# Kernel tuning notes

Hardware: AMD Instinct MI355X
Metric: run time of the kernel (lower is better)

## Reference

```python
import jax, jax.numpy as jnp
import numpy as np

TEMPERATURE = 0.1
BATCH_SIZE = 64
EPS = 1e-8  # torch.nn.CosineSimilarity eps
NEG_INF = -1e30

B, C, D = 64, 16, 512  # batch, children per sample, feature dim


def setup_inputs() -> dict:
    key = jax.random.key(0)
    k1, k2, k3, k4 = jax.random.split(key, 4)
    children_is = jax.random.normal(k1, (B, C, D), dtype=jnp.float32)
    children_js = jax.random.normal(k2, (B, C, D), dtype=jnp.float32)
    partnet_ids = jnp.arange(B, dtype=jnp.int64 if jax.config.jax_enable_x64 else jnp.int32)
    neg_idx_j = jax.random.randint(k3, (B, B, C), 0, C)  # negatives drawn from children_js
    neg_idx_k = jax.random.randint(k4, (B, B, C), 0, C)  # negatives drawn from children_is
    return {
        "children_is": children_is,
        "children_js": children_js,
        "partnet_ids": partnet_ids,
        "neg_idx_j": neg_idx_j,
        "neg_idx_k": neg_idx_k,
    }


def _safe_norm(x, axis=-1):
    return jnp.maximum(jnp.sqrt(jnp.sum(x * x, axis=axis)), EPS)


def _ntxent(ci, cj, pids, nj, nk):
    b = ci.shape[0]
    fi = ci.reshape(b, -1)  # [B, L] flattened anchors
    fj = cj.reshape(b, -1)  # [B, L] flattened positives
    norm_i = _safe_norm(fi)

    # positive: cos(flat(children_i), flat(children_j[i])) / T
    pos = jnp.sum(fi * fj, axis=-1) / (norm_i * _safe_norm(fj))  # [B]

    src = jnp.arange(b)[None, :, None]  # broadcast source-sample index
    # gathered negatives: g*[i, j] = children_*[j, neg_idx[i, j]] flattened -> [B, B, L]
    gj = cj[src, nj].reshape(b, b, -1)
    gk = ci[src, nk].reshape(b, b, -1)

    sim_j = jnp.einsum('il,ijl->ij', fi, gj) / (norm_i[:, None] * _safe_norm(gj))
    sim_k = jnp.einsum('il,ijl->ij', fi, gk) / (norm_i[:, None] * _safe_norm(gk))

    # negative pair valid iff j != i and partnet ids differ
    eye = jnp.arange(b)
    mask = (eye[None, :] != eye[:, None]) & (pids[None, :] != pids[:, None])  # [B, B]

    logits = jnp.concatenate(
        [pos[:, None],
         jnp.where(mask, sim_j, NEG_INF),
         jnp.where(mask, sim_k, NEG_INF)], axis=1) / TEMPERATURE  # [B, 1+2B]

    # CrossEntropy with label 0, reduction='sum' over the batch of anchors
    loss = jnp.sum(-logits[:, 0] + jax.scipy.special.logsumexp(logits, axis=1))
    return loss / (2.0 * BATCH_SIZE)


def reference(children_is, children_js, partnet_ids, neg_idx_j, neg_idx_k):
    return _ntxent(children_is, children_js, partnet_ids, neg_idx_j, neg_idx_k)
```

## Files before the change

### kernel.cpp

```cpp
#include <hip/hip_runtime.h>
#include <math.h>

#define BB 64
#define CC 16
#define DD 512
#define LL 8192
#define EPSV 1e-8f
#define INVT 10.0f
#define NEGINF_T (-1e31f)

#define OFF_CIB 0u
#define OFF_CJB (1u << 20)
#define BASE2   (2u << 20)
#define OFF_N2I (BASE2)
#define OFF_N2J (BASE2 + 4096u)
#define OFF_POS (BASE2 + 8192u)
#define OFF_DJ  (BASE2 + 12288u)
#define OFF_DK  (BASE2 + 12288u + 16384u)
#define OFF_GJ  (BASE2 + 12288u + 32768u)
#define OFF_GK  (BASE2 + 12288u + 49152u)

typedef short bf16x8 __attribute__((ext_vector_type(8)));
typedef float f32x4  __attribute__((ext_vector_type(4)));

__device__ __forceinline__ float dot4(float4 a, float4 b) {
    return a.x * b.x + a.y * b.y + a.z * b.z + a.w * b.w;
}
__device__ __forceinline__ float wave_reduce(float v) {
    #pragma unroll
    for (int off = 32; off; off >>= 1) v += __shfl_down(v, off);
    return v;
}
__device__ __forceinline__ unsigned short f2bf(float f) {
    union { float f; unsigned u; } x; x.f = f;
    return (unsigned short)((x.u + 0x7fffu + ((x.u >> 16) & 1u)) >> 16);
}

__global__ __launch_bounds__(256) void ntx_prep(const float* __restrict__ ci,
                                                const float* __restrict__ cj,
                                                char* __restrict__ ws,
                                                float* __restrict__ out) {
    const int b = blockIdx.x, tid = threadIdx.x;
    const int wave = tid >> 6, lane = tid & 63;
    __shared__ float red[4];

    if (b < 512) {
        const int r  = b * 4 + wave;
        const int rr = r & 1023;
        const bool is_i = (r < 1024);
        const float* src = is_i ? ci : cj;
        unsigned short* dst = (unsigned short*)(ws + (is_i ? OFF_CIB : OFF_CJB));
        float4 v1 = ((const float4*)(src + rr * DD))[lane];
        float4 v2 = ((const float4*)(src + rr * DD))[64 + lane];
        float acc = wave_reduce(dot4(v1, v1) + dot4(v2, v2));
        if (lane == 0) ((float*)(ws + (is_i ? OFF_N2I : OFF_N2J)))[rr] = acc;
        ushort4 h1 = { f2bf(v1.x), f2bf(v1.y), f2bf(v1.z), f2bf(v1.w) };
        ushort4 h2 = { f2bf(v2.x), f2bf(v2.y), f2bf(v2.z), f2bf(v2.w) };
        ((ushort4*)(dst + rr * DD))[lane]      = h1;
        ((ushort4*)(dst + rr * DD))[64 + lane] = h2;
    } else {
        const int i = b - 512;
        if (b == 512 && tid == 0) out[0] = 0.f;
        const float4* fi = (const float4*)(ci + i * LL);
        const float4* fj = (const float4*)(cj + i * LL);
        float acc = 0.f;
        #pragma unroll
        for (int it = 0; it < 8; ++it) acc += dot4(fi[tid + 256 * it], fj[tid + 256 * it]);
        acc = wave_reduce(acc);
        if (lane == 0) red[wave] = acc;
        __syncthreads();
        if (tid == 0) ((float*)(ws + OFF_POS))[i] = red[0] + red[1] + red[2] + red[3];
    }
}

__global__ __launch_bounds__(256) void ntx_strip(const int* __restrict__ nj,
                                                 const int* __restrict__ nk,
                                                 char* __restrict__ ws) {
    const int b = blockIdx.x;
    const int i = b >> 2, q = b & 3;
    const int side = q >> 1, jh = q & 1;
    const int tid  = threadIdx.x;
    const int wave = tid >> 6, lane = tid & 63;
    const int quad = lane >> 4, lr = lane & 15;

    __shared__ float sS[16][512];

    const short* A  = (const short*)(ws + OFF_CIB) + i * CC * DD;
    const short* Bm = (const short*)(ws + (side ? OFF_CIB : OFF_CJB)) + jh * 512 * DD;

    f32x4 acc[8] = {};
    #pragma unroll
    for (int kk = 0; kk < 16; ++kk) {
        const int k = kk * 32 + quad * 8;
        bf16x8 av = *(const bf16x8*)(A + lr * DD + k);
        #pragma unroll
        for (int tt = 0; tt < 8; ++tt) {
            const int row = (wave * 8 + tt) * 16 + lr;
            bf16x8 bv = *(const bf16x8*)(Bm + row * DD + k);
            acc[tt] = __builtin_amdgcn_mfma_f32_16x16x32_bf16(av, bv, acc[tt], 0, 0, 0);
        }
    }
    #pragma unroll
    for (int tt = 0; tt < 8; ++tt) {
        const int t = wave * 8 + tt;
        #pragma unroll
        for (int r = 0; r < 4; ++r)
            sS[quad * 4 + r][t * 16 + lr] = acc[tt][r];
    }
    __syncthreads();

    const int jj = tid >> 3;
    const int g  = tid & 7;
    const int j  = jh * 32 + jj;
    const int* idxp = (side ? nk : nj) + (i * BB + j) * CC;
    const float* n2 = (const float*)(ws + (side ? OFF_N2I : OFF_N2J)) + j * CC;
    const int c0 = g * 2;
    const int x0 = idxp[c0], x1 = idxp[c0 + 1];
    float d  = sS[c0][jj * 16 + x0] + sS[c0 + 1][jj * 16 + x1];
    float gn = n2[x0] + n2[x1];
    d += __shfl_down(d, 4);  gn += __shfl_down(gn, 4);
    d += __shfl_down(d, 2);  gn += __shfl_down(gn, 2);
    d += __shfl_down(d, 1);  gn += __shfl_down(gn, 1);
    if (g == 0) {
        ((float*)(ws + (side ? OFF_DK : OFF_DJ)))[i * BB + j] = d;
        ((float*)(ws + (side ? OFF_GK : OFF_GJ)))[i * BB + j] = gn;
    }
}

__global__ __launch_bounds__(64) void ntx_final(const int* __restrict__ pids,
                                                const char* __restrict__ ws_c,
                                                float* __restrict__ out) {
    const int i = blockIdx.x, j = threadIdx.x;
    const float* n2i = (const float*)(ws_c + OFF_N2I);
    const float* n2j = (const float*)(ws_c + OFF_N2J);
    const float* pos = (const float*)(ws_c + OFF_POS);

    float si = 0.f, sjf = 0.f;
    #pragma unroll
    for (int c = 0; c < CC; ++c) { si += n2i[i * CC + c]; sjf += n2j[i * CC + c]; }
    const float ni = fmaxf(sqrtf(si), EPSV);
    const float l0 = pos[i] / (ni * fmaxf(sqrtf(sjf), EPSV)) * INVT;

    const float dj = ((const float*)(ws_c + OFF_DJ))[i * BB + j];
    const float dk = ((const float*)(ws_c + OFF_DK))[i * BB + j];
    const float gj = ((const float*)(ws_c + OFF_GJ))[i * BB + j];
    const float gk = ((const float*)(ws_c + OFF_GK))[i * BB + j];

    const bool valid = (j != i) && (pids[j] != pids[i]);
    float lj = NEGINF_T, lk = NEGINF_T;
    if (valid) {
        const float inv = INVT / ni;
        lj = dj / fmaxf(sqrtf(gj), EPSV) * inv;
        lk = dk / fmaxf(sqrtf(gk), EPSV) * inv;
    }

    float m = fmaxf(lj, lk);
    #pragma unroll
    for (int off = 32; off; off >>= 1) m = fmaxf(m, __shfl_xor(m, off));
    m = fmaxf(m, l0);

    float s = __expf(lj - m) + __expf(lk - m);
    s = wave_reduce(s);
    if (j == 0) {
        s += __expf(l0 - m);
        const float loss_i = -l0 + m + __logf(s);
        atomicAdd(out, loss_i * (1.0f / (2.0f * BB)));
    }
}

extern "C" void kernel_launch(void* const* d_in, const int* in_sizes, int n_in,
                              void* d_out, int out_size, void* d_ws, size_t ws_size,
                              hipStream_t stream) {
    const float* ci  = (const float*)d_in[0];
    const float* cj  = (const float*)d_in[1];
    const int*  pids = (const int*) d_in[2];
    const int*  nj   = (const int*) d_in[3];
    const int*  nk   = (const int*) d_in[4];
    char*  ws  = (char*)d_ws;
    float* out = (float*)d_out;

    ntx_prep<<<576, 256, 0, stream>>>(ci, cj, ws, out);
    ntx_strip<<<256, 256, 0, stream>>>(nj, nk, ws);
    ntx_final<<<BB, 64, 0, stream>>>(pids, ws, out);
}
```

Baseline: 86.47 us.

## Fold final loss into strip kernel via last-block counter; fuse positive dot into prep

The separate final kernel is removed. The loss reduction now runs in the last of the four strip blocks per anchor, detected with an atomic counter plus threadfence. The prep kernel handles ci and cj rows together, computing per-row norms, the per-row positive dot product and the bf16 conversion in one pass, so the separate positive-dot blocks are no longer needed. This saves a kernel launch and a pass over the inputs, at the cost of atomic counter traffic and a workspace counter that prep must zero.

```diff
diff --git a/kernel.cpp b/kernel.cpp
--- a/kernel.cpp
+++ b/kernel.cpp
@@ -14,11 +14,12 @@
 #define BASE2   (2u << 20)
 #define OFF_N2I (BASE2)
 #define OFF_N2J (BASE2 + 4096u)
-#define OFF_POS (BASE2 + 8192u)
+#define OFF_PR  (BASE2 + 8192u)
 #define OFF_DJ  (BASE2 + 12288u)
-#define OFF_DK  (BASE2 + 12288u + 16384u)
-#define OFF_GJ  (BASE2 + 12288u + 32768u)
-#define OFF_GK  (BASE2 + 12288u + 49152u)
+#define OFF_DK  (BASE2 + 28672u)
+#define OFF_GJ  (BASE2 + 45056u)
+#define OFF_GK  (BASE2 + 61440u)
+#define OFF_CNT (BASE2 + 77824u)
 
 typedef short bf16x8 __attribute__((ext_vector_type(8)));
 typedef float f32x4  __attribute__((ext_vector_type(4)));
@@ -42,40 +43,42 @@
                                                 float* __restrict__ out) {
     const int b = blockIdx.x, tid = threadIdx.x;
     const int wave = tid >> 6, lane = tid & 63;
-    __shared__ float red[4];
-
-    if (b < 512) {
-        const int r  = b * 4 + wave;
-        const int rr = r & 1023;
-        const bool is_i = (r < 1024);
-        const float* src = is_i ? ci : cj;
-        unsigned short* dst = (unsigned short*)(ws + (is_i ? OFF_CIB : OFF_CJB));
-        float4 v1 = ((const float4*)(src + rr * DD))[lane];
-        float4 v2 = ((const float4*)(src + rr * DD))[64 + lane];
-        float acc = wave_reduce(dot4(v1, v1) + dot4(v2, v2));
-        if (lane == 0) ((float*)(ws + (is_i ? OFF_N2I : OFF_N2J)))[rr] = acc;
-        ushort4 h1 = { f2bf(v1.x), f2bf(v1.y), f2bf(v1.z), f2bf(v1.w) };
-        ushort4 h2 = { f2bf(v2.x), f2bf(v2.y), f2bf(v2.z), f2bf(v2.w) };
-        ((ushort4*)(dst + rr * DD))[lane]      = h1;
-        ((ushort4*)(dst + rr * DD))[64 + lane] = h2;
-    } else {
-        const int i = b - 512;
-        if (b == 512 && tid == 0) out[0] = 0.f;
-        const float4* fi = (const float4*)(ci + i * LL);
-        const float4* fj = (const float4*)(cj + i * LL);
-        float acc = 0.f;
-        #pragma unroll
-        for (int it = 0; it < 8; ++it) acc += dot4(fi[tid + 256 * it], fj[tid + 256 * it]);
-        acc = wave_reduce(acc);
-        if (lane == 0) red[wave] = acc;
-        __syncthreads();
-        if (tid == 0) ((float*)(ws + OFF_POS))[i] = red[0] + red[1] + red[2] + red[3];
+    const int r = b * 4 + wave;
+
+    const float4* ci4 = (const float4*)(ci + r * DD);
+    const float4* cj4 = (const float4*)(cj + r * DD);
+    float4 a1 = ci4[lane], a2 = ci4[64 + lane];
+    float4 b1 = cj4[lane], b2 = cj4[64 + lane];
+
+    float ni = wave_reduce(dot4(a1, a1) + dot4(a2, a2));
+    float nj = wave_reduce(dot4(b1, b1) + dot4(b2, b2));
+    float pd = wave_reduce(dot4(a1, b1) + dot4(a2, b2));
+    if (lane == 0) {
+        ((float*)(ws + OFF_N2I))[r] = ni;
+        ((float*)(ws + OFF_N2J))[r] = nj;
+        ((float*)(ws + OFF_PR))[r]  = pd;
+    }
+
+    ushort4 hi1 = { f2bf(a1.x), f2bf(a1.y), f2bf(a1.z), f2bf(a1.w) };
+    ushort4 hi2 = { f2bf(a2.x), f2bf(a2.y), f2bf(a2.z), f2bf(a2.w) };
+    ushort4 hj1 = { f2bf(b1.x), f2bf(b1.y), f2bf(b1.z), f2bf(b1.w) };
+    ushort4 hj2 = { f2bf(b2.x), f2bf(b2.y), f2bf(b2.z), f2bf(b2.w) };
+    ushort4* di = (ushort4*)((unsigned short*)(ws + OFF_CIB) + r * DD);
+    ushort4* dj = (ushort4*)((unsigned short*)(ws + OFF_CJB) + r * DD);
+    di[lane] = hi1;  di[64 + lane] = hi2;
+    dj[lane] = hj1;  dj[64 + lane] = hj2;
+
+    if (b == 0) {
+        if (tid < 64)       ((int*)(ws + OFF_CNT))[tid] = 0;
+        else if (tid == 64) out[0] = 0.f;
     }
 }
 
 __global__ __launch_bounds__(256) void ntx_strip(const int* __restrict__ nj,
                                                  const int* __restrict__ nk,
-                                                 char* __restrict__ ws) {
+                                                 const int* __restrict__ pids,
+                                                 char* __restrict__ ws,
+                                                 float* __restrict__ out) {
     const int b = blockIdx.x;
     const int i = b >> 2, q = b & 3;
     const int side = q >> 1, jh = q & 1;
@@ -84,6 +87,7 @@
     const int quad = lane >> 4, lr = lane & 15;
 
     __shared__ float sS[16][512];
+    __shared__ int   sOld;
 
     const short* A  = (const short*)(ws + OFF_CIB) + i * CC * DD;
     const short* Bm = (const short*)(ws + (side ? OFF_CIB : OFF_CJB)) + jh * 512 * DD;
@@ -109,62 +113,75 @@
     }
     __syncthreads();
 
-    const int jj = tid >> 3;
-    const int g  = tid & 7;
-    const int j  = jh * 32 + jj;
-    const int* idxp = (side ? nk : nj) + (i * BB + j) * CC;
-    const float* n2 = (const float*)(ws + (side ? OFF_N2I : OFF_N2J)) + j * CC;
-    const int c0 = g * 2;
-    const int x0 = idxp[c0], x1 = idxp[c0 + 1];
-    float d  = sS[c0][jj * 16 + x0] + sS[c0 + 1][jj * 16 + x1];
-    float gn = n2[x0] + n2[x1];
-    d += __shfl_down(d, 4);  gn += __shfl_down(gn, 4);
-    d += __shfl_down(d, 2);  gn += __shfl_down(gn, 2);
-    d += __shfl_down(d, 1);  gn += __shfl_down(gn, 1);
-    if (g == 0) {
-        ((float*)(ws + (side ? OFF_DK : OFF_DJ)))[i * BB + j] = d;
-        ((float*)(ws + (side ? OFF_GK : OFF_GJ)))[i * BB + j] = gn;
-    }
-}
-
-__global__ __launch_bounds__(64) void ntx_final(const int* __restrict__ pids,
-                                                const char* __restrict__ ws_c,
-                                                float* __restrict__ out) {
-    const int i = blockIdx.x, j = threadIdx.x;
-    const float* n2i = (const float*)(ws_c + OFF_N2I);
-    const float* n2j = (const float*)(ws_c + OFF_N2J);
-    const float* pos = (const float*)(ws_c + OFF_POS);
-
-    float si = 0.f, sjf = 0.f;
-    #pragma unroll
-    for (int c = 0; c < CC; ++c) { si += n2i[i * CC + c]; sjf += n2j[i * CC + c]; }
-    const float ni = fmaxf(sqrtf(si), EPSV);
-    const float l0 = pos[i] / (ni * fmaxf(sqrtf(sjf), EPSV)) * INVT;
-
-    const float dj = ((const float*)(ws_c + OFF_DJ))[i * BB + j];
-    const float dk = ((const float*)(ws_c + OFF_DK))[i * BB + j];
-    const float gj = ((const float*)(ws_c + OFF_GJ))[i * BB + j];
-    const float gk = ((const float*)(ws_c + OFF_GK))[i * BB + j];
-
-    const bool valid = (j != i) && (pids[j] != pids[i]);
-    float lj = NEGINF_T, lk = NEGINF_T;
-    if (valid) {
-        const float inv = INVT / ni;
-        lj = dj / fmaxf(sqrtf(gj), EPSV) * inv;
-        lk = dk / fmaxf(sqrtf(gk), EPSV) * inv;
-    }
-
-    float m = fmaxf(lj, lk);
-    #pragma unroll
-    for (int off = 32; off; off >>= 1) m = fmaxf(m, __shfl_xor(m, off));
-    m = fmaxf(m, l0);
-
-    float s = __expf(lj - m) + __expf(lk - m);
-    s = wave_reduce(s);
-    if (j == 0) {
-        s += __expf(l0 - m);
-        const float loss_i = -l0 + m + __logf(s);
-        atomicAdd(out, loss_i * (1.0f / (2.0f * BB)));
+    {
+        const int jj = tid >> 3;
+        const int g  = tid & 7;
+        const int j  = jh * 32 + jj;
+        const int* idxp = (side ? nk : nj) + (i * BB + j) * CC;
+        const float* n2 = (const float*)(ws + (side ? OFF_N2I : OFF_N2J)) + j * CC;
+        const int c0 = g * 2;
+        const int x0 = idxp[c0], x1 = idxp[c0 + 1];
+        float d  = sS[c0][jj * 16 + x0] + sS[c0 + 1][jj * 16 + x1];
+        float gn = n2[x0] + n2[x1];
+        d += __shfl_down(d, 4);  gn += __shfl_down(gn, 4);
+        d += __shfl_down(d, 2);  gn += __shfl_down(gn, 2);
+        d += __shfl_down(d, 1);  gn += __shfl_down(gn, 1);
+        if (g == 0) {
+            ((float*)(ws + (side ? OFF_DK : OFF_DJ)))[i * BB + j] = d;
+            ((float*)(ws + (side ? OFF_GK : OFF_GJ)))[i * BB + j] = gn;
+        }
+    }
+
+    __threadfence();
+    __syncthreads();
+    if (tid == 0) sOld = atomicAdd((int*)(ws + OFF_CNT) + i, 1);
+    __syncthreads();
+    if (sOld == 3 && tid < 64) {
+        const int j = tid;
+        __threadfence();
+        float* DJ = (float*)(ws + OFF_DJ);
+        float* DK = (float*)(ws + OFF_DK);
+        float* GJ = (float*)(ws + OFF_GJ);
+        float* GK = (float*)(ws + OFF_GK);
+        const float dj = atomicAdd(DJ + i * BB + j, 0.f);
+        const float dk = atomicAdd(DK + i * BB + j, 0.f);
+        const float gj = atomicAdd(GJ + i * BB + j, 0.f);
+        const float gk = atomicAdd(GK + i * BB + j, 0.f);
+
+        const float* n2i = (const float*)(ws + OFF_N2I);
+        const float* n2j = (const float*)(ws + OFF_N2J);
+        const float* pr  = (const float*)(ws + OFF_PR);
+        float si = 0.f, sjf = 0.f, pos = 0.f;
+        #pragma unroll
+        for (int c = 0; c < CC; ++c) {
+            si  += n2i[i * CC + c];
+            sjf += n2j[i * CC + c];
+            pos += pr[i * CC + c];
+        }
+        const float ni = fmaxf(sqrtf(si), EPSV);
+        const float l0 = pos / (ni * fmaxf(sqrtf(sjf), EPSV)) * INVT;
+
+        const bool valid = (j != i) && (pids[j] != pids[i]);
+        float lj = NEGINF_T, lk = NEGINF_T;
+        if (valid) {
+            const float inv = INVT / ni;
+            lj = dj / fmaxf(sqrtf(gj), EPSV) * inv;
+            lk = dk / fmaxf(sqrtf(gk), EPSV) * inv;
+        }
+
+        float m = fmaxf(lj, lk);
+        #pragma unroll
+        for (int off = 32; off; off >>= 1) m = fmaxf(m, __shfl_xor(m, off));
+        m = fmaxf(m, l0);
+
+        float s = __expf(lj - m) + __expf(lk - m);
+        #pragma unroll
+        for (int off = 32; off; off >>= 1) s += __shfl_down(s, off);
+        if (j == 0) {
+            s += __expf(l0 - m);
+            const float loss_i = -l0 + m + __logf(s);
+            atomicAdd(out, loss_i * (1.0f / (2.0f * BB)));
+        }
     }
 }
 
@@ -179,7 +196,6 @@
     char*  ws  = (char*)d_ws;
     float* out = (float*)d_out;
 
-    ntx_prep<<<576, 256, 0, stream>>>(ci, cj, ws, out);
-    ntx_strip<<<256, 256, 0, stream>>>(nj, nk, ws);
-    ntx_final<<<BB, 64, 0, stream>>>(pids, ws, out);
-}
+    ntx_prep<<<256, 256, 0, stream>>>(ci, cj, ws, out);
+    ntx_strip<<<256, 256, 0, stream>>>(nj, nk, pids, ws, out);
+}
```

New measurement: 99.90 us. 1.16x slower.
